# Kernel tuning notes

Measured on AMD Instinct MI355X. Metric: run time of the kernel, lower is better.

Reference implementation:

```python
import jax, jax.numpy as jnp
import numpy as np

N, E, H, D, FE = 50000, 400000, 4, 64, 64  # nodes, edges, heads, per-head dim, edge feat dim
NEG_SLOPE = 0.2


def setup_inputs() -> dict:
    key = jax.random.key(0)
    ks = jax.random.split(key, 18)
    def p(k, shape, s=0.1):
        return jax.random.normal(k, shape, dtype=jnp.float32) * s
    return dict(
        features=p(ks[0], (N, D), 1.0),
        edge_feat=p(ks[1], (E, FE), 1.0),
        src=jax.random.randint(ks[2], (E,), 0, N),
        dst=jax.random.randint(ks[3], (E,), 0, N),
        # layer 0: in=64 -> H*D=256, residual Linear since 64 != 256
        W0=p(ks[4], (D, H * D)), We0=p(ks[5], (FE, H * D)),
        al0=p(ks[6], (H, D)), ar0=p(ks[7], (H, D)), ae0=p(ks[8], (H, D)),
        b0=p(ks[9], (H * D,)), Wres0=p(ks[10], (D, H * D)),
        # layer 1 (last): in=256 -> H*D=256, residual = identity view
        W1=p(ks[11], (H * D, H * D)), We1=p(ks[12], (FE, H * D)),
        al1=p(ks[13], (H, D)), ar1=p(ks[14], (H, D)), ae1=p(ks[15], (H, D)),
        b1=p(ks[16], (H * D,)),
    )


def _edge_gat_layer(h, ef, src, dst, W, We, al, ar, ae, b, Wres=None):
    n = h.shape[0]
    ft = (h @ W).reshape(n, H, D)          # (N,H,D) projected node feats
    fe = (ef @ We).reshape(-1, H, D)       # (E,H,D) projected edge feats
    el = jnp.sum(ft * al, axis=-1)         # (N,H)
    er = jnp.sum(ft * ar, axis=-1)         # (N,H)
    ee = jnp.sum(fe * ae, axis=-1)         # (E,H)
    e = el[src] + er[dst] + ee             # (E,H)
    e = jnp.where(e > 0, e, NEG_SLOPE * e)  # leaky_relu(0.2)
    # segment softmax over incoming edges of each dst node
    m = jax.ops.segment_max(jax.lax.stop_gradient(e), dst, num_segments=n)
    ex = jnp.exp(e - m[dst])
    den = jax.ops.segment_sum(ex, dst, num_segments=n)
    a = ex / den[dst]                      # (E,H) attention
    out = jax.ops.segment_sum(ft[src] * a[:, :, None], dst, num_segments=n)  # (N,H,D)
    res = (h @ Wres).reshape(n, H, D) if Wres is not None else h.reshape(n, H, D)
    return out + res + b.reshape(1, H, D)


def reference(features, edge_feat, src, dst,
              W0, We0, al0, ar0, ae0, b0, Wres0,
              W1, We1, al1, ar1, ae1, b1):
    h = _edge_gat_layer(features, edge_feat, src, dst, W0, We0, al0, ar0, ae0, b0, Wres0)
    h = jax.nn.elu(h.reshape(N, H * D))    # flatten heads + ELU between layers
    h = _edge_gat_layer(h, edge_feat, src, dst, W1, We1, al1, ar1, ae1, b1)
    return h.mean(axis=1)                  # (N, D) mean over heads on last layer
```

## Files before the change

### kernel.cpp

```cpp
#include <hip/hip_runtime.h>
#include <hip/hip_bf16.h>

#define NN 50000
#define EE 400000

typedef __bf16 bf16_8 __attribute__((ext_vector_type(8)));
typedef float f32x4 __attribute__((ext_vector_type(4)));

__global__ __launch_bounds__(256) void scan1_kernel(const int* __restrict__ cnt,
                                                    int* __restrict__ scanbuf,
                                                    int* __restrict__ blocksum) {
  __shared__ int s[256];
  int t = threadIdx.x;
  int idx = blockIdx.x * 256 + t;
  int c = (idx < NN) ? cnt[idx] : 0;
  s[t] = c;
  __syncthreads();
  for (int d = 1; d < 256; d <<= 1) {
    int v = (t >= d) ? s[t - d] : 0;
    __syncthreads();
    s[t] += v;
    __syncthreads();
  }
  if (idx < NN) scanbuf[idx] = s[t];
  if (t == 255) blocksum[blockIdx.x] = s[255];
}

__global__ __launch_bounds__(256) void scan2_kernel(const int* __restrict__ blocksum,
                                                    int* __restrict__ blockoff, int nb) {
  __shared__ int s[256];
  int t = threadIdx.x;
  int c = (t < nb) ? blocksum[t] : 0;
  s[t] = c;
  __syncthreads();
  for (int d = 1; d < 256; d <<= 1) {
    int v = (t >= d) ? s[t - d] : 0;
    __syncthreads();
    s[t] += v;
    __syncthreads();
  }
  if (t < nb) blockoff[t] = s[t] - c;
}

__global__ __launch_bounds__(256) void scan3_kernel(const int* __restrict__ scanbuf,
                                                    const int* __restrict__ cnt,
                                                    const int* __restrict__ blockoff,
                                                    int* __restrict__ off,
                                                    int* __restrict__ cur) {
  int idx = blockIdx.x * 256 + threadIdx.x;
  if (idx < NN) {
    int o = blockoff[blockIdx.x] + scanbuf[idx] - cnt[idx];
    off[idx] = o;
    cur[idx] = o;
  }
  if (idx == 0) off[NN] = EE;
}

__global__ __launch_bounds__(256) void fill_kernel(const int* __restrict__ src,
                                                   const int* __restrict__ dst,
                                                   int* __restrict__ cur,
                                                   int* __restrict__ pos,
                                                   int* __restrict__ srcc,
                                                   int* __restrict__ dstc) {
  int e = blockIdx.x * 256 + threadIdx.x;
  if (e < EE) {
    int d = dst[e];
    int p = atomicAdd(&cur[d], 1);
    pos[e] = p;
    srcc[p] = src[e];
    dstc[p] = d;
  }
}

__global__ __launch_bounds__(256) void prep_kernel(
    const float* __restrict__ features, __bf16* __restrict__ fbf,
    const float* __restrict__ W0, const float* __restrict__ Wres0, __bf16* __restrict__ Bt0,
    const float* __restrict__ W1, __bf16* __restrict__ Bt1,
    const float* __restrict__ We0, const float* __restrict__ ae0, float* __restrict__ Ve0,
    const float* __restrict__ We1, const float* __restrict__ ae1, float* __restrict__ Ve1,
    const int* __restrict__ dst, int* __restrict__ cnt) {
  int b = blockIdx.x;
  int t = threadIdx.x;
  if (b < 1563) {
    int i = b * 256 + t;
    if (i < NN * 64 / 8) {
      const float4* p = (const float4*)features + (size_t)i * 2;
      float4 a = p[0], c = p[1];
      bf16_8 v = {(__bf16)a.x, (__bf16)a.y, (__bf16)a.z, (__bf16)a.w,
                  (__bf16)c.x, (__bf16)c.y, (__bf16)c.z, (__bf16)c.w};
      *(bf16_8*)(fbf + (size_t)i * 8) = v;
    }
  } else if (b < 1563 + 128) {
    int idx = (b - 1563) * 256 + t;
    int j = idx >> 6, k = idx & 63;
    float v = (j < 256) ? W0[k * 256 + j] : Wres0[k * 256 + (j - 256)];
    Bt0[idx] = (__bf16)v;
  } else if (b < 1563 + 128 + 256) {
    int idx = (b - 1563 - 128) * 256 + t;
    int j = idx >> 8, k = idx & 255;
    Bt1[idx] = (__bf16)W1[k * 256 + j];
  } else if (b == 1947) {
    int f = t >> 2, h = t & 3;
    float s = 0.f;
    for (int d = 0; d < 64; ++d) s += We0[f * 256 + h * 64 + d] * ae0[h * 64 + d];
    Ve0[f * 4 + h] = s;
  } else if (b == 1948) {
    int f = t >> 2, h = t & 3;
    float s = 0.f;
    for (int d = 0; d < 64; ++d) s += We1[f * 256 + h * 64 + d] * ae1[h * 64 + d];
    Ve1[f * 4 + h] = s;
  } else {
    int e = (b - 1949) * 256 + t;
    if (e < EE) atomicAdd(&cnt[dst[e]], 1);
  }
}

#define LDK 40
__global__ __launch_bounds__(256) void gemm_kernel(const __bf16* __restrict__ A,
                                                   const __bf16* __restrict__ Bt,
                                                   __bf16* __restrict__ ft,
                                                   __bf16* __restrict__ base,
                                                   const float* __restrict__ bias,
                                                   const float* __restrict__ al,
                                                   const float* __restrict__ ar,
                                                   float* __restrict__ el,
                                                   float* __restrict__ er,
                                                   int M, int K) {
  __shared__ __align__(16) __bf16 Al[64 * LDK];
  __shared__ __align__(16) __bf16 Bl[64 * LDK];
  int tid = threadIdx.x;
  int wav = tid >> 6, lane = tid & 63;
  int quad = lane >> 4, l16 = lane & 15;
  int bm = blockIdx.x * 64;
  int bn = blockIdx.y * 64;
  int sr = tid >> 2;
  int sk = (tid & 3) << 3;

  f32x4 acc[4] = {{0, 0, 0, 0}, {0, 0, 0, 0}, {0, 0, 0, 0}, {0, 0, 0, 0}};

  for (int k0 = 0; k0 < K; k0 += 32) {
    uint4 av = {0, 0, 0, 0};
    int arow = bm + sr;
    if (arow < M) av = *(const uint4*)(A + (size_t)arow * K + k0 + sk);
    uint4 bv = *(const uint4*)(Bt + (size_t)(bn + sr) * K + k0 + sk);
    __syncthreads();
    *(uint4*)&Al[sr * LDK + sk] = av;
    *(uint4*)&Bl[sr * LDK + sk] = bv;
    __syncthreads();
    bf16_8 af = *(const bf16_8*)&Al[(wav * 16 + l16) * LDK + quad * 8];
#pragma unroll
    for (int nt = 0; nt < 4; ++nt) {
      bf16_8 bf = *(const bf16_8*)&Bl[(nt * 16 + l16) * LDK + quad * 8];
      acc[nt] = __builtin_amdgcn_mfma_f32_16x16x32_bf16(af, bf, acc[nt], 0, 0, 0);
    }
  }

  int row0 = bm + wav * 16 + quad * 4;

  if (bn < 256) {
    int hb = bn >> 6;
#pragma unroll
    for (int r = 0; r < 4; ++r) {
      float pl = 0.f, pr = 0.f;
#pragma unroll
      for (int nt = 0; nt < 4; ++nt) {
        float v = acc[nt][r];
        int d = nt * 16 + l16;
        pl += v * al[hb * 64 + d];
        pr += v * ar[hb * 64 + d];
      }
#pragma unroll
      for (int o2 = 8; o2 > 0; o2 >>= 1) {
        pl += __shfl_xor(pl, o2);
        pr += __shfl_xor(pr, o2);
      }
      int row = row0 + r;
      if (l16 == 0 && row < M) {
        el[row * 4 + hb] = pl;
        er[row * 4 + hb] = pr;
      }
    }
  }

#pragma unroll
  for (int nt = 0; nt < 4; ++nt) {
    int col = bn + nt * 16 + l16;
#pragma unroll
    for (int r = 0; r < 4; ++r) {
      int row = row0 + r;
      if (row < M) {
        float v = acc[nt][r];
        if (col < 256)
          ft[(size_t)row * 256 + col] = (__bf16)v;
        else
          base[(size_t)row * 256 + (col - 256)] = (__bf16)(v + bias[col - 256]);
      }
    }
  }
}

__global__ __launch_bounds__(256) void edge0_kernel(const float* __restrict__ ef,
                                                    const int* __restrict__ src,
                                                    const int* __restrict__ dst,
                                                    const int* __restrict__ pos,
                                                    const float* __restrict__ Ve0,
                                                    const float* __restrict__ Ve1,
                                                    const float* __restrict__ el,
                                                    const float* __restrict__ er,
                                                    float* __restrict__ esc,
                                                    float* __restrict__ ee1c) {
  __shared__ float V0[256], V1[256];
  V0[threadIdx.x] = Ve0[threadIdx.x];
  V1[threadIdx.x] = Ve1[threadIdx.x];
  __syncthreads();
  int e = blockIdx.x * 256 + threadIdx.x;
  if (e >= EE) return;
  float a0 = 0, a1 = 0, a2 = 0, a3 = 0;
  float c0 = 0, c1 = 0, c2 = 0, c3 = 0;
  const float* row = ef + (size_t)e * 64;
#pragma unroll
  for (int i0 = 0; i0 < 64; i0 += 4) {
    float4 v = *(const float4*)(row + i0);
    float xs[4] = {v.x, v.y, v.z, v.w};
#pragma unroll
    for (int j = 0; j < 4; ++j) {
      float x = xs[j];
      const float* p0 = &V0[(i0 + j) * 4];
      const float* p1 = &V1[(i0 + j) * 4];
      a0 += x * p0[0]; a1 += x * p0[1]; a2 += x * p0[2]; a3 += x * p0[3];
      c0 += x * p1[0]; c1 += x * p1[1]; c2 += x * p1[2]; c3 += x * p1[3];
    }
  }
  int s = src[e], d = dst[e];
  float4 l = *(const float4*)(el + (size_t)s * 4);
  float4 r = *(const float4*)(er + (size_t)d * 4);
  float4 o;
  o.x = l.x + r.x + a0;
  o.y = l.y + r.y + a1;
  o.z = l.z + r.z + a2;
  o.w = l.w + r.w + a3;
  o.x = __expf(o.x > 0.f ? o.x : 0.2f * o.x);
  o.y = __expf(o.y > 0.f ? o.y : 0.2f * o.y);
  o.z = __expf(o.z > 0.f ? o.z : 0.2f * o.z);
  o.w = __expf(o.w > 0.f ? o.w : 0.2f * o.w);
  int p = pos[e];
  *(float4*)(esc + (size_t)p * 4) = o;
  float4 c;
  c.x = c0; c.y = c1; c.z = c2; c.w = c3;
  *(float4*)(ee1c + (size_t)p * 4) = c;
}

__global__ __launch_bounds__(256) void edge1_kernel(const int* __restrict__ srcc,
                                                    const int* __restrict__ dstc,
                                                    const float* __restrict__ ee1c,
                                                    const float* __restrict__ el,
                                                    const float* __restrict__ er,
                                                    float* __restrict__ esc) {
  int p = blockIdx.x * 256 + threadIdx.x;
  if (p >= EE) return;
  int s = srcc[p], d = dstc[p];
  float4 c = *(const float4*)(ee1c + (size_t)p * 4);
  float4 l = *(const float4*)(el + (size_t)s * 4);
  float4 r = *(const float4*)(er + (size_t)d * 4);
  float4 o;
  o.x = l.x + r.x + c.x;
  o.y = l.y + r.y + c.y;
  o.z = l.z + r.z + c.z;
  o.w = l.w + r.w + c.w;
  o.x = __expf(o.x > 0.f ? o.x : 0.2f * o.x);
  o.y = __expf(o.y > 0.f ? o.y : 0.2f * o.y);
  o.z = __expf(o.z > 0.f ? o.z : 0.2f * o.z);
  o.w = __expf(o.w > 0.f ? o.w : 0.2f * o.w);
  *(float4*)(esc + (size_t)p * 4) = o;
}

template <int LAYER>
__global__ __launch_bounds__(256) void agg_kernel(const int* __restrict__ off,
                                                  const int* __restrict__ srcc,
                                                  const float* __restrict__ esc,
                                                  const __bf16* __restrict__ ft,
                                                  const __bf16* prev,
                                                  const float* __restrict__ bias,
                                                  __bf16* outb,
                                                  float* __restrict__ outf) {
  __shared__ float red[256];
  int n = blockIdx.x;
  int t = threadIdx.x, h = t >> 6, lane = t & 63;
  int beg = off[n], end = off[n + 1];
  float pv = (float)prev[(size_t)n * 256 + t];
  float bv = (LAYER == 1) ? bias[t] : 0.f;
  int offd = h * 64 + lane;

  float acc = 0.f, den = 0.f;
  int j = beg;
  for (; j + 4 <= end; j += 4) {
    int s0 = srcc[j], s1 = srcc[j + 1], s2 = srcc[j + 2], s3 = srcc[j + 3];
    float w0 = esc[(size_t)(j + 0) * 4 + h];
    float w1 = esc[(size_t)(j + 1) * 4 + h];
    float w2 = esc[(size_t)(j + 2) * 4 + h];
    float w3 = esc[(size_t)(j + 3) * 4 + h];
    float v0 = (float)ft[(size_t)s0 * 256 + offd];
    float v1 = (float)ft[(size_t)s1 * 256 + offd];
    float v2 = (float)ft[(size_t)s2 * 256 + offd];
    float v3 = (float)ft[(size_t)s3 * 256 + offd];
    acc += w0 * v0; acc += w1 * v1; acc += w2 * v2; acc += w3 * v3;
    den += w0 + w1 + w2 + w3;
  }
  for (; j < end; ++j) {
    float w = esc[(size_t)j * 4 + h];
    acc += w * (float)ft[(size_t)srcc[j] * 256 + offd];
    den += w;
  }
  float res = (end > beg) ? acc / den : 0.f;

  if (LAYER == 0) {
    float v = res + pv;
    v = v > 0.f ? v : (__expf(v) - 1.0f);
    outb[(size_t)n * 256 + t] = (__bf16)v;
  } else {
    red[t] = res + pv + bv;
    __syncthreads();
    if (t < 64)
      outf[(size_t)n * 64 + t] =
          0.25f * (red[t] + red[t + 64] + red[t + 128] + red[t + 192]);
  }
}

extern "C" void kernel_launch(void* const* d_in, const int* in_sizes, int n_in,
                              void* d_out, int out_size, void* d_ws, size_t ws_size,
                              hipStream_t stream) {
  const float* features  = (const float*)d_in[0];
  const float* edge_feat = (const float*)d_in[1];
  const int*   src       = (const int*)d_in[2];
  const int*   dst       = (const int*)d_in[3];
  const float* W0    = (const float*)d_in[4];
  const float* We0   = (const float*)d_in[5];
  const float* al0   = (const float*)d_in[6];
  const float* ar0   = (const float*)d_in[7];
  const float* ae0   = (const float*)d_in[8];
  const float* b0    = (const float*)d_in[9];
  const float* Wres0 = (const float*)d_in[10];
  const float* W1    = (const float*)d_in[11];
  const float* We1   = (const float*)d_in[12];
  const float* al1   = (const float*)d_in[13];
  const float* ar1   = (const float*)d_in[14];
  const float* ae1   = (const float*)d_in[15];
  const float* b1    = (const float*)d_in[16];
  float* out = (float*)d_out;

  char* ws = (char*)d_ws;
  size_t o = 0;
  auto alloc = [&](size_t bytes) {
    void* p = ws + o;
    o = (o + bytes + 255) & ~(size_t)255;
    return p;
  };
  int*    cnt      = (int*)alloc((size_t)NN * 4);
  int*    scanbuf  = (int*)alloc((size_t)NN * 4);
  int*    blocksum = (int*)alloc(256 * 4);
  int*    blockoff = (int*)alloc(256 * 4);
  int*    off      = (int*)alloc((size_t)(NN + 1) * 4);
  int*    cur      = (int*)alloc((size_t)NN * 4);
  int*    pos      = (int*)alloc((size_t)EE * 4);
  int*    srcc     = (int*)alloc((size_t)EE * 4);
  int*    dstc     = (int*)alloc((size_t)EE * 4);
  float*  esc      = (float*)alloc((size_t)EE * 4 * 4);
  float*  ee1c     = (float*)alloc((size_t)EE * 4 * 4);
  float*  el       = (float*)alloc((size_t)NN * 4 * 4);
  float*  er       = (float*)alloc((size_t)NN * 4 * 4);
  float*  Ve0      = (float*)alloc(256 * 4);
  float*  Ve1      = (float*)alloc(256 * 4);
  __bf16* Bt0      = (__bf16*)alloc((size_t)512 * 64 * 2);
  __bf16* Bt1      = (__bf16*)alloc((size_t)256 * 256 * 2);
  __bf16* fbf      = (__bf16*)alloc((size_t)NN * 64 * 2);
  __bf16* ft       = (__bf16*)alloc((size_t)NN * 256 * 2);
  __bf16* base     = (__bf16*)alloc((size_t)NN * 256 * 2);
  __bf16* h1       = base;

  const int EB = (EE + 255) / 256;
  const int NB = (NN + 255) / 256;
  const int MG = (NN + 63) / 64;

  hipMemsetAsync(cnt, 0, (size_t)NN * 4, stream);
  prep_kernel<<<1949 + EB, 256, 0, stream>>>(features, fbf, W0, Wres0, Bt0, W1, Bt1,
                                             We0, ae0, Ve0, We1, ae1, Ve1, dst, cnt);
  scan1_kernel<<<NB, 256, 0, stream>>>(cnt, scanbuf, blocksum);
  scan2_kernel<<<1, 256, 0, stream>>>(blocksum, blockoff, NB);
  scan3_kernel<<<NB, 256, 0, stream>>>(scanbuf, cnt, blockoff, off, cur);
  fill_kernel<<<EB, 256, 0, stream>>>(src, dst, cur, pos, srcc, dstc);

  gemm_kernel<<<dim3(MG, 8), 256, 0, stream>>>(fbf, Bt0, ft, base, b0, al0, ar0, el, er, NN, 64);
  edge0_kernel<<<EB, 256, 0, stream>>>(edge_feat, src, dst, pos, Ve0, Ve1, el, er, esc, ee1c);
  agg_kernel<0><<<NN, 256, 0, stream>>>(off, srcc, esc, ft, base, nullptr, h1, nullptr);

  gemm_kernel<<<dim3(MG, 4), 256, 0, stream>>>(h1, Bt1, ft, nullptr, nullptr, al1, ar1, el, er, NN, 256);
  edge1_kernel<<<EB, 256, 0, stream>>>(srcc, dstc, ee1c, el, er, esc);
  agg_kernel<1><<<NN, 256, 0, stream>>>(off, srcc, esc, ft, h1, b1, nullptr, out);
}
```

Before: 458.3 us.

## Fuse edge score computation into aggregation and use single-pass decoupled scan

Replaces the three-kernel prefix scan with a single-pass scan that chains block offsets through flags and uses a ticket to order blocks. The edge-feature projection becomes a separate eek kernel that uses four threads per edge and a shuffle reduction. Both edge-score kernels are removed: the aggregation now recomputes leaky-relu and exp per edge from el, er and the projected edge features, reached through an edge-id indirection. This drops two edge passes and the esc/ee1c arrays, but adds gathers and redundant exp work in the aggregation, since each of the 64 lanes per head repeats them.

```diff
diff --git a/kernel.cpp b/kernel.cpp
--- a/kernel.cpp
+++ b/kernel.cpp
@@ -3,74 +3,10 @@
 
 #define NN 50000
 #define EE 400000
+#define NB 196
 
 typedef __bf16 bf16_8 __attribute__((ext_vector_type(8)));
 typedef float f32x4 __attribute__((ext_vector_type(4)));
-
-__global__ __launch_bounds__(256) void scan1_kernel(const int* __restrict__ cnt,
-                                                    int* __restrict__ scanbuf,
-                                                    int* __restrict__ blocksum) {
-  __shared__ int s[256];
-  int t = threadIdx.x;
-  int idx = blockIdx.x * 256 + t;
-  int c = (idx < NN) ? cnt[idx] : 0;
-  s[t] = c;
-  __syncthreads();
-  for (int d = 1; d < 256; d <<= 1) {
-    int v = (t >= d) ? s[t - d] : 0;
-    __syncthreads();
-    s[t] += v;
-    __syncthreads();
-  }
-  if (idx < NN) scanbuf[idx] = s[t];
-  if (t == 255) blocksum[blockIdx.x] = s[255];
-}
-
-__global__ __launch_bounds__(256) void scan2_kernel(const int* __restrict__ blocksum,
-                                                    int* __restrict__ blockoff, int nb) {
-  __shared__ int s[256];
-  int t = threadIdx.x;
-  int c = (t < nb) ? blocksum[t] : 0;
-  s[t] = c;
-  __syncthreads();
-  for (int d = 1; d < 256; d <<= 1) {
-    int v = (t >= d) ? s[t - d] : 0;
-    __syncthreads();
-    s[t] += v;
-    __syncthreads();
-  }
-  if (t < nb) blockoff[t] = s[t] - c;
-}
-
-__global__ __launch_bounds__(256) void scan3_kernel(const int* __restrict__ scanbuf,
-                                                    const int* __restrict__ cnt,
-                                                    const int* __restrict__ blockoff,
-                                                    int* __restrict__ off,
-                                                    int* __restrict__ cur) {
-  int idx = blockIdx.x * 256 + threadIdx.x;
-  if (idx < NN) {
-    int o = blockoff[blockIdx.x] + scanbuf[idx] - cnt[idx];
-    off[idx] = o;
-    cur[idx] = o;
-  }
-  if (idx == 0) off[NN] = EE;
-}
-
-__global__ __launch_bounds__(256) void fill_kernel(const int* __restrict__ src,
-                                                   const int* __restrict__ dst,
-                                                   int* __restrict__ cur,
-                                                   int* __restrict__ pos,
-                                                   int* __restrict__ srcc,
-                                                   int* __restrict__ dstc) {
-  int e = blockIdx.x * 256 + threadIdx.x;
-  if (e < EE) {
-    int d = dst[e];
-    int p = atomicAdd(&cur[d], 1);
-    pos[e] = p;
-    srcc[p] = src[e];
-    dstc[p] = d;
-  }
-}
 
 __global__ __launch_bounds__(256) void prep_kernel(
     const float* __restrict__ features, __bf16* __restrict__ fbf,
@@ -115,6 +51,106 @@
   }
 }
 
+__global__ __launch_bounds__(256) void cscan_kernel(const int* __restrict__ cnt,
+                                                    int* __restrict__ off,
+                                                    int* __restrict__ cur,
+                                                    int* __restrict__ ticket,
+                                                    int* __restrict__ flag) {
+  __shared__ int s[256];
+  __shared__ int sbid, sbase;
+  int t = threadIdx.x;
+  if (t == 0) sbid = atomicAdd(ticket, 1);
+  __syncthreads();
+  int bid = sbid;
+  int idx = bid * 256 + t;
+  int c = (idx < NN) ? cnt[idx] : 0;
+  s[t] = c;
+  __syncthreads();
+  for (int d = 1; d < 256; d <<= 1) {
+    int v = (t >= d) ? s[t - d] : 0;
+    __syncthreads();
+    s[t] += v;
+    __syncthreads();
+  }
+  if (t == 0) {
+    int base = 0;
+    if (bid > 0) {
+      int v;
+      do {
+        v = __hip_atomic_load(&flag[bid - 1], __ATOMIC_ACQUIRE, __HIP_MEMORY_SCOPE_AGENT);
+      } while (v == 0);
+      base = v - 1;
+    }
+    __hip_atomic_store(&flag[bid], base + s[255] + 1, __ATOMIC_RELEASE,
+                       __HIP_MEMORY_SCOPE_AGENT);
+    sbase = base;
+  }
+  __syncthreads();
+  int base = sbase;
+  if (idx < NN) {
+    int o = base + s[t] - c;
+    off[idx] = o;
+    cur[idx] = o;
+  }
+  if (idx == 0) off[NN] = EE;
+}
+
+__global__ __launch_bounds__(256) void fill_kernel(const int* __restrict__ src,
+                                                   const int* __restrict__ dst,
+                                                   int* __restrict__ cur,
+                                                   int* __restrict__ srcc,
+                                                   int* __restrict__ eidc) {
+  int e = blockIdx.x * 256 + threadIdx.x;
+  if (e < EE) {
+    int p = atomicAdd(&cur[dst[e]], 1);
+    srcc[p] = src[e];
+    eidc[p] = e;
+  }
+}
+
+__global__ __launch_bounds__(256) void eek_kernel(const float* __restrict__ ef,
+                                                  const float* __restrict__ Ve0,
+                                                  const float* __restrict__ Ve1,
+                                                  float* __restrict__ eeo) {
+  __shared__ float V0[256], V1[256];
+  V0[threadIdx.x] = Ve0[threadIdx.x];
+  V1[threadIdx.x] = Ve1[threadIdx.x];
+  __syncthreads();
+  int r = threadIdx.x >> 2, sub = threadIdx.x & 3;
+  int e = blockIdx.x * 64 + r;
+  if (e >= EE) return;
+  float a0 = 0, a1 = 0, a2 = 0, a3 = 0;
+  float c0 = 0, c1 = 0, c2 = 0, c3 = 0;
+  const float* row = ef + (size_t)e * 64 + sub * 16;
+#pragma unroll
+  for (int i = 0; i < 16; i += 4) {
+    float4 v = *(const float4*)(row + i);
+    float xs[4] = {v.x, v.y, v.z, v.w};
+#pragma unroll
+    for (int j = 0; j < 4; ++j) {
+      float x = xs[j];
+      int idx = (sub * 16 + i + j) * 4;
+      a0 += x * V0[idx + 0]; a1 += x * V0[idx + 1];
+      a2 += x * V0[idx + 2]; a3 += x * V0[idx + 3];
+      c0 += x * V1[idx + 0]; c1 += x * V1[idx + 1];
+      c2 += x * V1[idx + 2]; c3 += x * V1[idx + 3];
+    }
+  }
+#pragma unroll
+  for (int o = 1; o < 4; o <<= 1) {
+    a0 += __shfl_xor(a0, o); a1 += __shfl_xor(a1, o);
+    a2 += __shfl_xor(a2, o); a3 += __shfl_xor(a3, o);
+    c0 += __shfl_xor(c0, o); c1 += __shfl_xor(c1, o);
+    c2 += __shfl_xor(c2, o); c3 += __shfl_xor(c3, o);
+  }
+  if (sub == 0) {
+    float4 u; u.x = a0; u.y = a1; u.z = a2; u.w = a3;
+    float4 w; w.x = c0; w.y = c1; w.z = c2; w.w = c3;
+    *(float4*)(eeo + (size_t)e * 8) = u;
+    *(float4*)(eeo + (size_t)e * 8 + 4) = w;
+  }
+}
+
 #define LDK 40
 __global__ __launch_bounds__(256) void gemm_kernel(const __bf16* __restrict__ A,
                                                    const __bf16* __restrict__ Bt,
@@ -199,85 +235,13 @@
   }
 }
 
-__global__ __launch_bounds__(256) void edge0_kernel(const float* __restrict__ ef,
-                                                    const int* __restrict__ src,
-                                                    const int* __restrict__ dst,
-                                                    const int* __restrict__ pos,
-                                                    const float* __restrict__ Ve0,
-                                                    const float* __restrict__ Ve1,
-                                                    const float* __restrict__ el,
-                                                    const float* __restrict__ er,
-                                                    float* __restrict__ esc,
-                                                    float* __restrict__ ee1c) {
-  __shared__ float V0[256], V1[256];
-  V0[threadIdx.x] = Ve0[threadIdx.x];
-  V1[threadIdx.x] = Ve1[threadIdx.x];
-  __syncthreads();
-  int e = blockIdx.x * 256 + threadIdx.x;
-  if (e >= EE) return;
-  float a0 = 0, a1 = 0, a2 = 0, a3 = 0;
-  float c0 = 0, c1 = 0, c2 = 0, c3 = 0;
-  const float* row = ef + (size_t)e * 64;
-#pragma unroll
-  for (int i0 = 0; i0 < 64; i0 += 4) {
-    float4 v = *(const float4*)(row + i0);
-    float xs[4] = {v.x, v.y, v.z, v.w};
-#pragma unroll
-    for (int j = 0; j < 4; ++j) {
-      float x = xs[j];
-      const float* p0 = &V0[(i0 + j) * 4];
-      const float* p1 = &V1[(i0 + j) * 4];
-      a0 += x * p0[0]; a1 += x * p0[1]; a2 += x * p0[2]; a3 += x * p0[3];
-      c0 += x * p1[0]; c1 += x * p1[1]; c2 += x * p1[2]; c3 += x * p1[3];
-    }
-  }
-  int s = src[e], d = dst[e];
-  float4 l = *(const float4*)(el + (size_t)s * 4);
-  float4 r = *(const float4*)(er + (size_t)d * 4);
-  float4 o;
-  o.x = l.x + r.x + a0;
-  o.y = l.y + r.y + a1;
-  o.z = l.z + r.z + a2;
-  o.w = l.w + r.w + a3;
-  o.x = __expf(o.x > 0.f ? o.x : 0.2f * o.x);
-  o.y = __expf(o.y > 0.f ? o.y : 0.2f * o.y);
-  o.z = __expf(o.z > 0.f ? o.z : 0.2f * o.z);
-  o.w = __expf(o.w > 0.f ? o.w : 0.2f * o.w);
-  int p = pos[e];
-  *(float4*)(esc + (size_t)p * 4) = o;
-  float4 c;
-  c.x = c0; c.y = c1; c.z = c2; c.w = c3;
-  *(float4*)(ee1c + (size_t)p * 4) = c;
-}
-
-__global__ __launch_bounds__(256) void edge1_kernel(const int* __restrict__ srcc,
-                                                    const int* __restrict__ dstc,
-                                                    const float* __restrict__ ee1c,
-                                                    const float* __restrict__ el,
-                                                    const float* __restrict__ er,
-                                                    float* __restrict__ esc) {
-  int p = blockIdx.x * 256 + threadIdx.x;
-  if (p >= EE) return;
-  int s = srcc[p], d = dstc[p];
-  float4 c = *(const float4*)(ee1c + (size_t)p * 4);
-  float4 l = *(const float4*)(el + (size_t)s * 4);
-  float4 r = *(const float4*)(er + (size_t)d * 4);
-  float4 o;
-  o.x = l.x + r.x + c.x;
-  o.y = l.y + r.y + c.y;
-  o.z = l.z + r.z + c.z;
-  o.w = l.w + r.w + c.w;
-  o.x = __expf(o.x > 0.f ? o.x : 0.2f * o.x);
-  o.y = __expf(o.y > 0.f ? o.y : 0.2f * o.y);
-  o.z = __expf(o.z > 0.f ? o.z : 0.2f * o.z);
-  o.w = __expf(o.w > 0.f ? o.w : 0.2f * o.w);
-  *(float4*)(esc + (size_t)p * 4) = o;
-}
-
 template <int LAYER>
 __global__ __launch_bounds__(256) void agg_kernel(const int* __restrict__ off,
                                                   const int* __restrict__ srcc,
-                                                  const float* __restrict__ esc,
+                                                  const int* __restrict__ eidc,
+                                                  const float* __restrict__ eeo,
+                                                  const float* __restrict__ el,
+                                                  const float* __restrict__ er,
                                                   const __bf16* __restrict__ ft,
                                                   const __bf16* prev,
                                                   const float* __restrict__ bias,
@@ -289,16 +253,22 @@
   int beg = off[n], end = off[n + 1];
   float pv = (float)prev[(size_t)n * 256 + t];
   float bv = (LAYER == 1) ? bias[t] : 0.f;
+  float ern = er[n * 4 + h];
   int offd = h * 64 + lane;
 
   float acc = 0.f, den = 0.f;
   int j = beg;
   for (; j + 4 <= end; j += 4) {
     int s0 = srcc[j], s1 = srcc[j + 1], s2 = srcc[j + 2], s3 = srcc[j + 3];
-    float w0 = esc[(size_t)(j + 0) * 4 + h];
-    float w1 = esc[(size_t)(j + 1) * 4 + h];
-    float w2 = esc[(size_t)(j + 2) * 4 + h];
-    float w3 = esc[(size_t)(j + 3) * 4 + h];
+    int e0 = eidc[j], e1 = eidc[j + 1], e2 = eidc[j + 2], e3 = eidc[j + 3];
+    float z0 = el[s0 * 4 + h] + ern + eeo[(size_t)e0 * 8 + LAYER * 4 + h];
+    float z1 = el[s1 * 4 + h] + ern + eeo[(size_t)e1 * 8 + LAYER * 4 + h];
+    float z2 = el[s2 * 4 + h] + ern + eeo[(size_t)e2 * 8 + LAYER * 4 + h];
+    float z3 = el[s3 * 4 + h] + ern + eeo[(size_t)e3 * 8 + LAYER * 4 + h];
+    float w0 = __expf(z0 > 0.f ? z0 : 0.2f * z0);
+    float w1 = __expf(z1 > 0.f ? z1 : 0.2f * z1);
+    float w2 = __expf(z2 > 0.f ? z2 : 0.2f * z2);
+    float w3 = __expf(z3 > 0.f ? z3 : 0.2f * z3);
     float v0 = (float)ft[(size_t)s0 * 256 + offd];
     float v1 = (float)ft[(size_t)s1 * 256 + offd];
     float v2 = (float)ft[(size_t)s2 * 256 + offd];
@@ -307,8 +277,10 @@
     den += w0 + w1 + w2 + w3;
   }
   for (; j < end; ++j) {
-    float w = esc[(size_t)j * 4 + h];
-    acc += w * (float)ft[(size_t)srcc[j] * 256 + offd];
+    int s = srcc[j];
+    float z = el[s * 4 + h] + ern + eeo[(size_t)eidc[j] * 8 + LAYER * 4 + h];
+    float w = __expf(z > 0.f ? z : 0.2f * z);
+    acc += w * (float)ft[(size_t)s * 256 + offd];
     den += w;
   }
   float res = (end > beg) ? acc / den : 0.f;
@@ -356,16 +328,14 @@
     return p;
   };
   int*    cnt      = (int*)alloc((size_t)NN * 4);
-  int*    scanbuf  = (int*)alloc((size_t)NN * 4);
-  int*    blocksum = (int*)alloc(256 * 4);
-  int*    blockoff = (int*)alloc(256 * 4);
+  int*    ticket   = (int*)alloc(64 * 4);
+  int*    flag     = (int*)alloc((size_t)NB * 4);
+  size_t  zbytes   = (size_t)((char*)flag + NB * 4 - (char*)cnt);
   int*    off      = (int*)alloc((size_t)(NN + 1) * 4);
   int*    cur      = (int*)alloc((size_t)NN * 4);
-  int*    pos      = (int*)alloc((size_t)EE * 4);
   int*    srcc     = (int*)alloc((size_t)EE * 4);
-  int*    dstc     = (int*)alloc((size_t)EE * 4);
-  float*  esc      = (float*)alloc((size_t)EE * 4 * 4);
-  float*  ee1c     = (float*)alloc((size_t)EE * 4 * 4);
+  int*    eidc     = (int*)alloc((size_t)EE * 4);
+  float*  eeo      = (float*)alloc((size_t)EE * 8 * 4);
   float*  el       = (float*)alloc((size_t)NN * 4 * 4);
   float*  er       = (float*)alloc((size_t)NN * 4 * 4);
   float*  Ve0      = (float*)alloc(256 * 4);
@@ -378,22 +348,18 @@
   __bf16* h1       = base;
 
   const int EB = (EE + 255) / 256;
-  const int NB = (NN + 255) / 256;
   const int MG = (NN + 63) / 64;
 
-  hipMemsetAsync(cnt, 0, (size_t)NN * 4, stream);
+  hipMemsetAsync(cnt, 0, zbytes, stream);
   prep_kernel<<<1949 + EB, 256, 0, stream>>>(features, fbf, W0, Wres0, Bt0, W1, Bt1,
                                              We0, ae0, Ve0, We1, ae1, Ve1, dst, cnt);
-  scan1_kernel<<<NB, 256, 0, stream>>>(cnt, scanbuf, blocksum);
-  scan2_kernel<<<1, 256, 0, stream>>>(blocksum, blockoff, NB);
-  scan3_kernel<<<NB, 256, 0, stream>>>(scanbuf, cnt, blockoff, off, cur);
-  fill_kernel<<<EB, 256, 0, stream>>>(src, dst, cur, pos, srcc, dstc);
+  cscan_kernel<<<NB, 256, 0, stream>>>(cnt, off, cur, ticket, flag);
+  fill_kernel<<<EB, 256, 0, stream>>>(src, dst, cur, srcc, eidc);
+  eek_kernel<<<(EE + 63) / 64, 256, 0, stream>>>(edge_feat, Ve0, Ve1, eeo);
 
   gemm_kernel<<<dim3(MG, 8), 256, 0, stream>>>(fbf, Bt0, ft, base, b0, al0, ar0, el, er, NN, 64);
-  edge0_kernel<<<EB, 256, 0, stream>>>(edge_feat, src, dst, pos, Ve0, Ve1, el, er, esc, ee1c);
-  agg_kernel<0><<<NN, 256, 0, stream>>>(off, srcc, esc, ft, base, nullptr, h1, nullptr);
+  agg_kernel<0><<<NN, 256, 0, stream>>>(off, srcc, eidc, eeo, el, er, ft, base, nullptr, h1, nullptr);
 
   gemm_kernel<<<dim3(MG, 4), 256, 0, stream>>>(h1, Bt1, ft, nullptr, nullptr, al1, ar1, el, er, NN, 256);
-  edge1_kernel<<<EB, 256, 0, stream>>>(srcc, dstc, ee1c, el, er, esc);
-  agg_kernel<1><<<NN, 256, 0, stream>>>(off, srcc, esc, ft, h1, b1, nullptr, out);
-}
+  agg_kernel<1><<<NN, 256, 0, stream>>>(off, srcc, eidc, eeo, el, er, ft, h1, b1, nullptr, out);
+}
```

Result: slower. 801.8 us (+75.0%).
